# Kernel tuning notes

Measured on AMD Instinct MI355X. Metric: run time of the kernel, lower is better.

## Reference

```python
import jax, jax.numpy as jnp
import numpy as np

H = 4  # attention heads


def gat_layer(x, src, dst, W, a_src, a_dst, b, N):
    """PyG-style GATConv (concat=True, negative_slope=0.2, eval-mode dropout)."""
    h = (x @ W).reshape(N, H, -1)                       # [N,H,C]
    es = jnp.einsum('nhc,hc->nh', h, a_src)             # per-node src score
    ed = jnp.einsum('nhc,hc->nh', h, a_dst)             # per-node dst score
    e = jax.nn.leaky_relu(es[src] + ed[dst], negative_slope=0.2)  # [E,H]
    # segment softmax over incoming edges of each destination node
    emax = jax.ops.segment_max(e, dst, num_segments=N)
    ee = jnp.exp(e - emax[dst])
    denom = jax.ops.segment_sum(ee, dst, num_segments=N)
    alpha = ee / (denom[dst] + 1e-16)                   # [E,H]
    out = jax.ops.segment_sum(h[src] * alpha[..., None], dst, num_segments=N)
    return out.reshape(N, -1) + b                        # [N,H*C]


def setup_inputs() -> dict:
    key = jax.random.key(0)
    ks = jax.random.split(key, 13)
    N, E, D, Q = 50000, 800000, 256, 8
    HID, OUT = 256, 256
    Ch, Co = HID // H, OUT // H
    inp = {}
    inp['x'] = jax.random.normal(ks[0], (N, D), dtype=jnp.float32)
    inp['edge_index'] = jax.random.randint(ks[1], (2, E), 0, N, dtype=jnp.int64)
    inp['query_embedding'] = jax.random.normal(ks[2], (Q, OUT), dtype=jnp.float32)
    # layer 1: input_dim -> heads * (hidden_dim//heads)
    inp['W1'] = jax.random.normal(ks[3], (D, HID), dtype=jnp.float32) / np.sqrt(D).astype(np.float32)
    inp['a_src1'] = jax.random.normal(ks[4], (H, Ch), dtype=jnp.float32) / np.sqrt(Ch).astype(np.float32)
    inp['a_dst1'] = jax.random.normal(ks[5], (H, Ch), dtype=jnp.float32) / np.sqrt(Ch).astype(np.float32)
    inp['b1'] = jnp.zeros((HID,), dtype=jnp.float32)
    # layer 2: hidden_dim -> heads * (output_dim//heads)
    inp['W2'] = jax.random.normal(ks[6], (HID, OUT), dtype=jnp.float32) / np.sqrt(HID).astype(np.float32)
    inp['a_src2'] = jax.random.normal(ks[7], (H, Co), dtype=jnp.float32) / np.sqrt(Co).astype(np.float32)
    inp['a_dst2'] = jax.random.normal(ks[8], (H, Co), dtype=jnp.float32) / np.sqrt(Co).astype(np.float32)
    inp['b2'] = jnp.zeros((OUT,), dtype=jnp.float32)
    # node classifier over concat([query, node]) -> 1 (intended Linear(2*OUT, 1))
    inp['Wc'] = jax.random.normal(ks[9], (2 * OUT, 1), dtype=jnp.float32) / np.sqrt(2 * OUT).astype(np.float32)
    inp['bc'] = jnp.zeros((1,), dtype=jnp.float32)
    return inp


def reference(x, edge_index, query_embedding, W1, a_src1, a_dst1, b1,
              W2, a_src2, a_dst2, b2, Wc, bc):
    N = x.shape[0]
    loops = jnp.arange(N, dtype=edge_index.dtype)        # GATConv add_self_loops=True
    src = jnp.concatenate([edge_index[0], loops])
    dst = jnp.concatenate([edge_index[1], loops])
    h = jax.nn.relu(gat_layer(x, src, dst, W1, a_src1, a_dst1, b1, N))
    emb = gat_layer(h, src, dst, W2, a_src2, a_dst2, b2, N)  # [N, OUT]
    D = emb.shape[1]
    # scores[q,n] = Linear(concat(query[q], emb[n])) — computed without
    # materializing the [Q,N,2D] concat (identical math).
    q_part = query_embedding @ Wc[:D] + bc               # [Q,1]
    n_part = emb @ Wc[D:]                                # [N,1]
    node_scores = q_part[:, 0][:, None] + n_part[:, 0][None, :]  # [Q,N]
    return emb, node_scores
```

## Files before the change

kernel.cpp:

```cpp
#include <hip/hip_runtime.h>

typedef unsigned short u16;
typedef unsigned int   u32;
typedef __attribute__((ext_vector_type(8))) short short8v;
typedef __attribute__((ext_vector_type(8))) unsigned short us8;
typedef __attribute__((ext_vector_type(4))) float f32x4;

static __device__ __forceinline__ float bf2f(u16 u){ union{u32 i; float f;} v; v.i=(u32)u<<16; return v.f; }
static __device__ __forceinline__ u16 f2bf(float f){ union{float f; u32 i;} u; u.f=f; u32 r=u.i+0x7FFFu+((u.i>>16)&1u); return (u16)(r>>16); }

static __device__ __forceinline__ float ld1(const void* p, size_t i, int f32){
  return f32 ? ((const float*)p)[i] : bf2f(((const u16*)p)[i]);
}
static __device__ __forceinline__ float4 ld4(const void* p, size_t i, int f32){
  if (f32) return *((const float4*)((const float*)p + i));
  ushort4 v = *((const ushort4*)((const u16*)p + i));
  return make_float4(bf2f(v.x), bf2f(v.y), bf2f(v.z), bf2f(v.w));
}
static __device__ __forceinline__ void st4(void* p, size_t i, float4 v, int f32){
  if (f32) *((float4*)((float*)p + i)) = v;
  else { ushort4 o; o.x=f2bf(v.x); o.y=f2bf(v.y); o.z=f2bf(v.z); o.w=f2bf(v.w); *((ushort4*)((u16*)p + i)) = o; }
}
static __device__ __forceinline__ void st1(void* p, size_t i, float v, int f32){
  if (f32) ((float*)p)[i] = v; else ((u16*)p)[i] = f2bf(v);
}
static __device__ __forceinline__ int lde(const int* ei, size_t i, int i64){
  return i64 ? ei[2*i] : ei[i];
}
static __device__ __forceinline__ int clampi(int v, int lo, int hi){ return v<lo?lo:(v>hi?hi:v); }

__global__ void detect_zero_kernel(const u32* __restrict__ x, const int* __restrict__ ei,
                                   int* __restrict__ flags, int* __restrict__ deg, int N){
  if (blockIdx.x != 0){
    int i = (blockIdx.x - 1)*256 + threadIdx.x;
    if (i < N) deg[i] = 0;
    return;
  }
  __shared__ int cnt[2];
  int t = threadIdx.x;
  if (t < 2) cnt[t] = 0;
  __syncthreads();
  int good = 0;
  for (int i = t; i < 4096; i += 256){
    u32 e = (x[i] >> 7) & 0xFFu;
    if (e >= 90u && e <= 150u) good++;
  }
  atomicAdd(&cnt[0], good);
  int nzodd = 0;
  for (int i = t; i < 2048; i += 256){
    if (ei[2*i+1] != 0) nzodd++;
  }
  atomicAdd(&cnt[1], nzodd);
  __syncthreads();
  if (t == 0){
    flags[0] = (cnt[0] < 2867) ? 1 : 0;
    flags[1] = (cnt[1] == 0) ? 1 : 0;
  }
}

__global__ void count_kernel(const int* __restrict__ ei, int E, int N,
                             int* __restrict__ deg, const int* __restrict__ flags){
  int i64 = flags[1];
  int i = blockIdx.x*blockDim.x + threadIdx.x;
  int Et = E + N;
  if (i < Et){
    int d = (i < E) ? clampi(lde(ei, (size_t)E + i, i64), 0, N-1) : (i - E);
    atomicAdd(&deg[d], 1);
  }
}

__global__ __launch_bounds__(256) void scan1_kernel(const int* __restrict__ deg,
    int* __restrict__ offs, int* __restrict__ bsum, int N){
  __shared__ int sm[256];
  int t = threadIdx.x;
  int i = blockIdx.x*256 + t;
  int v = (i < N) ? deg[i] : 0;
  sm[t] = v; __syncthreads();
  #pragma unroll
  for (int off = 1; off < 256; off <<= 1){
    int u = (t >= off) ? sm[t-off] : 0;
    __syncthreads();
    sm[t] += u;
    __syncthreads();
  }
  if (i < N) offs[i] = sm[t] - v;
  if (t == 255) bsum[blockIdx.x] = sm[255];
}

__global__ __launch_bounds__(1024) void scan2_kernel(const int* __restrict__ bsum,
    int* __restrict__ bpre, int NB){
  __shared__ int sm[1024];
  int t = threadIdx.x;
  int v = (t < NB) ? bsum[t] : 0;
  sm[t] = v; __syncthreads();
  #pragma unroll
  for (int off = 1; off < 1024; off <<= 1){
    int u = (t >= off) ? sm[t-off] : 0;
    __syncthreads();
    sm[t] += u;
    __syncthreads();
  }
  if (t < NB) bpre[t] = sm[t] - v;
  if (t == 1023) bpre[NB] = sm[1023];
}

__global__ __launch_bounds__(256) void scan3_kernel(int* __restrict__ offs,
    int* __restrict__ cursor, const int* __restrict__ bpre, int N, int NB){
  int i = blockIdx.x*256 + threadIdx.x;
  if (i < N){
    int v = offs[i] + bpre[blockIdx.x];
    offs[i] = v; cursor[i] = v;
  }
  if (i == 0) offs[N] = bpre[NB];
}

__global__ __launch_bounds__(256) void scatter_prep_kernel(const int* __restrict__ ei,
    int E, int N, int SB, int* __restrict__ cursor, int* __restrict__ csr_src,
    const void* __restrict__ B1, const void* __restrict__ B2,
    u16* __restrict__ BT1, u16* __restrict__ BT2,
    const void* __restrict__ query, const void* __restrict__ Wc, const void* __restrict__ bc,
    float* __restrict__ qp, int Q, const int* __restrict__ flags){
  int f32 = flags[0];
  int i64 = flags[1];
  int bid = blockIdx.x;
  if (bid < SB){
    int i = bid*256 + threadIdx.x;
    int Et = E + N;
    if (i < Et){
      int s, d;
      if (i < E){
        s = clampi(lde(ei, i, i64), 0, N-1);
        d = clampi(lde(ei, (size_t)E + i, i64), 0, N-1);
      } else { s = i - E; d = s; }
      int p = atomicAdd(&cursor[d], 1);
      csr_src[p] = s;
    }
    return;
  }
  int pb = bid - SB;
  if (pb < 32){
    const void* B = (pb >= 16) ? B2 : B1;
    u16* BT = (pb >= 16) ? BT2 : BT1;
    int rem = pb & 15;
    int k0 = (rem >> 2)*64, c0 = (rem & 3)*64;
    __shared__ u16 tile[64][65];
    int r0 = threadIdx.x >> 6, c = threadIdx.x & 63;
    for (int r = r0; r < 64; r += 4)
      tile[r][c] = f32 ? f2bf(((const float*)B)[(size_t)(k0+r)*256 + c0 + c])
                       : ((const u16*)B)[(size_t)(k0+r)*256 + c0 + c];
    __syncthreads();
    for (int j = r0; j < 64; j += 4)
      BT[(size_t)(c0+j)*256 + k0 + c] = tile[c][j];
  } else {
    int q = threadIdx.x >> 5, ln = threadIdx.x & 31;
    if (q >= Q) return;
    float s = 0.f;
    for (int j = ln; j < 256; j += 32) s += ld1(query, q*256 + j, f32) * ld1(Wc, j, f32);
    #pragma unroll
    for (int off = 16; off; off >>= 1) s += __shfl_down(s, off, 32);
    if (ln == 0) qp[q] = s + ld1(bc, 0, f32);
  }
}

__global__ __launch_bounds__(512, 4) void gemm_mfma(const void* __restrict__ A,
    const u16* __restrict__ BT, u16* __restrict__ C, int M, int aIsInput,
    const int* __restrict__ flags, float* __restrict__ es, float* __restrict__ ed,
    const void* __restrict__ a_src, const void* __restrict__ a_dst){
  int af32 = aIsInput ? flags[0] : 0;
  int f32 = flags[0];
  __shared__ __align__(16) u16 smem[128*40 + 256*40];
  u16* AsB = smem;
  u16* BsB = smem + 128*40;
  int tid = threadIdx.x;
  int wave = tid >> 6, lane = tid & 63;
  int wm = wave >> 2, wn = wave & 3;
  int l15 = lane & 15, l4 = lane >> 4;
  int row0 = blockIdx.x * 128;
  const u16*  A16 = (const u16*)A;
  const float* A32 = (const float*)A;
  int srow = tid >> 2, sks = (tid & 3) * 8;
  int scol = tid >> 1, skh = (tid & 1) * 16;
  int sgr = min(row0 + srow, M-1);
  f32x4 acc[4][4] = {};
  for (int k0 = 0; k0 < 256; k0 += 32){
    __syncthreads();
    {
      us8 av;
      if (af32){
        const float* ap = A32 + (size_t)sgr*256 + k0 + sks;
        float4 v0 = *(const float4*)ap, v1 = *(const float4*)(ap+4);
        av = (us8){f2bf(v0.x),f2bf(v0.y),f2bf(v0.z),f2bf(v0.w),
                   f2bf(v1.x),f2bf(v1.y),f2bf(v1.z),f2bf(v1.w)};
      } else {
        av = *(const us8*)(A16 + (size_t)sgr*256 + k0 + sks);
      }
      *(us8*)&AsB[srow*40 + sks] = av;
      const u16* bp = BT + (size_t)scol*256 + k0 + skh;
      *(us8*)&BsB[scol*40 + skh]     = *(const us8*)bp;
      *(us8*)&BsB[scol*40 + skh + 8] = *(const us8*)(bp + 8);
    }
    __syncthreads();
    short8v a[4], b[4];
    #pragma unroll
    for (int mi = 0; mi < 4; mi++)
      a[mi] = *(const short8v*)&AsB[(wm*64 + mi*16 + l15)*40 + 8*l4];
    #pragma unroll
    for (int ni = 0; ni < 4; ni++)
      b[ni] = *(const short8v*)&BsB[(wn*64 + ni*16 + l15)*40 + 8*l4];
    #pragma unroll
    for (int mi = 0; mi < 4; mi++)
      #pragma unroll
      for (int ni = 0; ni < 4; ni++)
        acc[mi][ni] = __builtin_amdgcn_mfma_f32_16x16x32_bf16(a[mi], b[ni], acc[mi][ni], 0, 0, 0);
  }
  float as_[4], ad_[4];
  #pragma unroll
  for (int ni = 0; ni < 4; ni++){
    as_[ni] = ld1(a_src, wn*64 + ni*16 + l15, f32);
    ad_[ni] = ld1(a_dst, wn*64 + ni*16 + l15, f32);
  }
  #pragma unroll
  for (int mi = 0; mi < 4; mi++){
    #pragma unroll
    for (int r = 0; r < 4; r++){
      float pe = acc[mi][0][r]*as_[0] + acc[mi][1][r]*as_[1]
               + acc[mi][2][r]*as_[2] + acc[mi][3][r]*as_[3];
      float pd = acc[mi][0][r]*ad_[0] + acc[mi][1][r]*ad_[1]
               + acc[mi][2][r]*ad_[2] + acc[mi][3][r]*ad_[3];
      #pragma unroll
      for (int off = 1; off < 16; off <<= 1){
        pe += __shfl_xor(pe, off, 64);
        pd += __shfl_xor(pd, off, 64);
      }
      if (l15 == 0){
        int row = row0 + wm*64 + mi*16 + l4*4 + r;
        if (row < M){
          es[(size_t)row*4 + wn] = pe;
          ed[(size_t)row*4 + wn] = pd;
        }
      }
    }
  }
  u16* tile = smem;
  __syncthreads();
  #pragma unroll
  for (int mi = 0; mi < 4; mi++){
    #pragma unroll
    for (int ni = 0; ni < 4; ni++)
      #pragma unroll
      for (int r = 0; r < 4; r++)
        tile[(wm*16 + l4*4 + r)*264 + wn*64 + ni*16 + l15] = f2bf(acc[mi][ni][r]);
    __syncthreads();
    #pragma unroll
    for (int c = tid; c < 1024; c += 512){
      int lr = c >> 5, col = (c & 31) * 8;
      int grow = row0 + (lr >> 4)*64 + mi*16 + (lr & 15);
      if (grow < M)
        *(us8*)&C[(size_t)grow*256 + col] = *(const us8*)&tile[lr*264 + col];
    }
    __syncthreads();
  }
}

__global__ __launch_bounds__(256) void agg_kernel(const u16* __restrict__ h,
    const int* __restrict__ csr_src, const int* __restrict__ offs,
    const float* __restrict__ es, const float* __restrict__ ed, int N,
    const void* __restrict__ bias, void* __restrict__ out, int do_relu, int outIsOutput,
    const int* __restrict__ flags, const void* __restrict__ Wc,
    const float* __restrict__ qp, int Q){
  int f32in = flags[0];
  int of32  = outIsOutput ? flags[0] : 0;
  int ln = threadIdx.x & 63;
  int n = blockIdx.x*4 + (threadIdx.x >> 6);
  if (n >= N) return;
  int beg = offs[n], end = offs[n+1];
  int hd = ln >> 4, c0 = ln*4;
  float edn = ed[(size_t)n*4 + hd];
  float a0=0.f, a1=0.f, a2=0.f, a3=0.f, ws=0.f;
  int i = beg;
  for (; i + 8 <= end; i += 8){
    int s[8]; float x[8]; ushort4 hv[8];
    #pragma unroll
    for (int j = 0; j < 8; j++) s[j] = csr_src[i+j];
    #pragma unroll
    for (int j = 0; j < 8; j++) x[j] = es[(size_t)s[j]*4 + hd];
    #pragma unroll
    for (int j = 0; j < 8; j++) hv[j] = *(const ushort4*)&h[(size_t)s[j]*256 + c0];
    #pragma unroll
    for (int j = 0; j < 8; j++){
      float t = x[j] + edn; t = (t > 0.f) ? t : 0.2f*t; t = fminf(t, 60.f);
      float w = __expf(t);
      a0 += w*bf2f(hv[j].x); a1 += w*bf2f(hv[j].y);
      a2 += w*bf2f(hv[j].z); a3 += w*bf2f(hv[j].w);
      ws += w;
    }
  }
  for (; i + 4 <= end; i += 4){
    int s[4]; float x[4]; ushort4 hv[4];
    #pragma unroll
    for (int j = 0; j < 4; j++) s[j] = csr_src[i+j];
    #pragma unroll
    for (int j = 0; j < 4; j++) x[j] = es[(size_t)s[j]*4 + hd];
    #pragma unroll
    for (int j = 0; j < 4; j++) hv[j] = *(const ushort4*)&h[(size_t)s[j]*256 + c0];
    #pragma unroll
    for (int j = 0; j < 4; j++){
      float t = x[j] + edn; t = (t > 0.f) ? t : 0.2f*t; t = fminf(t, 60.f);
      float w = __expf(t);
      a0 += w*bf2f(hv[j].x); a1 += w*bf2f(hv[j].y);
      a2 += w*bf2f(hv[j].z); a3 += w*bf2f(hv[j].w);
      ws += w;
    }
  }
  for (; i < end; i++){
    int s = csr_src[i];
    float t = es[(size_t)s*4 + hd] + edn; t = (t > 0.f) ? t : 0.2f*t; t = fminf(t, 60.f);
    float w = __expf(t);
    ushort4 hv = *(const ushort4*)&h[(size_t)s*256 + c0];
    a0 += w*bf2f(hv.x); a1 += w*bf2f(hv.y);
    a2 += w*bf2f(hv.z); a3 += w*bf2f(hv.w);
    ws += w;
  }
  float inv = 1.f / (ws + 1e-16f);
  float4 bv = ld4(bias, c0, f32in);
  float4 ov = make_float4(a0*inv + bv.x, a1*inv + bv.y, a2*inv + bv.z, a3*inv + bv.w);
  if (do_relu){
    ov.x = fmaxf(ov.x, 0.f); ov.y = fmaxf(ov.y, 0.f);
    ov.z = fmaxf(ov.z, 0.f); ov.w = fmaxf(ov.w, 0.f);
  }
  st4(out, (size_t)n*256 + c0, ov, of32);
  if (outIsOutput){
    float4 wc4 = ld4(Wc, 256 + c0, f32in);
    float v = ov.x*wc4.x + ov.y*wc4.y + ov.z*wc4.z + ov.w*wc4.w;
    #pragma unroll
    for (int off = 1; off < 64; off <<= 1) v += __shfl_xor(v, off, 64);
    if (ln < Q) st1(out, (size_t)N*256 + (size_t)ln*N + n, qp[ln] + v, of32);
  }
}

extern "C" void kernel_launch(void* const* d_in, const int* in_sizes, int n_in,
                              void* d_out, int out_size, void* d_ws, size_t ws_size,
                              hipStream_t stream){
  const void* x     = d_in[0];
  const int*  ei    = (const int*)d_in[1];
  const void* query = d_in[2];
  const void* W1    = d_in[3];
  const void* as1   = d_in[4];
  const void* ad1   = d_in[5];
  const void* b1    = d_in[6];
  const void* W2    = d_in[7];
  const void* as2   = d_in[8];
  const void* ad2   = d_in[9];
  const void* b2    = d_in[10];
  const void* Wc    = d_in[11];
  const void* bc    = d_in[12];

  int N = in_sizes[0] / 256;
  int E = in_sizes[1] / 2;
  int Q = in_sizes[2] / 256;
  int Et = E + N;
  int NB = (N + 255) / 256;
  int SB = (Et + 255) / 256;

  char* p = (char*)d_ws;
  auto alloc = [&](size_t bytes)->char*{
    char* r = p; p += (bytes + 255) & ~(size_t)255; return r;
  };
  int*  flags    = (int*) alloc(256);
  u16*  bufA     = (u16*) alloc((size_t)N*256*2);
  u16*  bufB     = (u16*) alloc((size_t)N*256*2);
  float* es      = (float*)alloc((size_t)N*4*4);
  float* ed      = (float*)alloc((size_t)N*4*4);
  int*  deg      = (int*)  alloc((size_t)N*4);
  int*  offs     = (int*)  alloc((size_t)(N+1)*4);
  int*  cursor   = (int*)  alloc((size_t)N*4);
  int*  csr_src  = (int*)  alloc((size_t)Et*4);
  int*  bsum     = (int*)  alloc((size_t)(NB+1)*4);
  int*  bpre     = (int*)  alloc((size_t)(NB+1)*4);
  u16*  BT1      = (u16*)  alloc(256*256*2);
  u16*  BT2      = (u16*)  alloc(256*256*2);
  float* qp      = (float*)alloc(64*4);

  const int thr = 256;
  detect_zero_kernel<<<NB + 1, 256, 0, stream>>>((const u32*)x, ei, flags, deg, N);
  count_kernel <<<(Et + thr-1)/thr, thr, 0, stream>>>(ei, E, N, deg, flags);
  scan1_kernel <<<NB, 256, 0, stream>>>(deg, offs, bsum, N);
  scan2_kernel <<<1, 1024, 0, stream>>>(bsum, bpre, NB);
  scan3_kernel <<<NB, 256, 0, stream>>>(offs, cursor, bpre, N, NB);
  scatter_prep_kernel<<<SB + 33, 256, 0, stream>>>(ei, E, N, SB, cursor, csr_src,
                                                   W1, W2, BT1, BT2, query, Wc, bc,
                                                   qp, Q, flags);

  int gblocks = (N + 127)/128;
  dim3 ngrid((N + 3)/4);

  gemm_mfma <<<gblocks, 512, 0, stream>>>(x, BT1, bufA, N, 1, flags, es, ed, as1, ad1);
  agg_kernel<<<ngrid, 256, 0, stream>>>(bufA, csr_src, offs, es, ed, N, b1, bufB, 1, 0,
                                        flags, Wc, qp, Q);
  gemm_mfma <<<gblocks, 512, 0, stream>>>(bufB, BT2, bufA, N, 0, flags, es, ed, as2, ad2);
  agg_kernel<<<ngrid, 256, 0, stream>>>(bufA, csr_src, offs, es, ed, N, b2, d_out, 0, 1,
                                        flags, Wc, qp, Q);
}
```

Measured before the change: 299.2 us.

## Precompute per-edge attention weights in CSR order before aggregation

Adds a csr_dst array filled during the scatter and a new edgew_kernel that computes exp(leaky_relu(es[src]+ed[dst])) for all four heads of every edge, storing them contiguously in CSR order. The aggregation kernel then reads these weights with a sequential load instead of gathering es per edge and recomputing the exponential in each of 16 lanes per head. This removes redundant exp work and scattered es loads from the aggregation loop. In exchange it adds an extra kernel launch per layer plus writing and re-reading roughly 13 MB of edge weights and the csr_dst array.

New measurement: 308.9 us. +3.2%, slower.

```diff
diff --git a/kernel.cpp b/kernel.cpp
--- a/kernel.cpp
+++ b/kernel.cpp
@@ -116,6 +116,7 @@
 
 __global__ __launch_bounds__(256) void scatter_prep_kernel(const int* __restrict__ ei,
     int E, int N, int SB, int* __restrict__ cursor, int* __restrict__ csr_src,
+    int* __restrict__ csr_dst,
     const void* __restrict__ B1, const void* __restrict__ B2,
     u16* __restrict__ BT1, u16* __restrict__ BT2,
     const void* __restrict__ query, const void* __restrict__ Wc, const void* __restrict__ bc,
@@ -134,6 +135,7 @@
       } else { s = i - E; d = s; }
       int p = atomicAdd(&cursor[d], 1);
       csr_src[p] = s;
+      csr_dst[p] = d;
     }
     return;
   }
@@ -160,6 +162,22 @@
     for (int off = 16; off; off >>= 1) s += __shfl_down(s, off, 32);
     if (ln == 0) qp[q] = s + ld1(bc, 0, f32);
   }
+}
+
+__global__ __launch_bounds__(256) void edgew_kernel(const int* __restrict__ csr_src,
+    const int* __restrict__ csr_dst, const float* __restrict__ es,
+    const float* __restrict__ ed, float* __restrict__ w_csr, int Et){
+  int i = blockIdx.x*256 + threadIdx.x;
+  if (i >= Et) return;
+  int s = csr_src[i], d = csr_dst[i];
+  float4 e1 = *(const float4*)&es[(size_t)s*4];
+  float4 e2 = *(const float4*)&ed[(size_t)d*4];
+  float4 o;
+  float t0 = e1.x + e2.x; t0 = (t0 > 0.f) ? t0 : 0.2f*t0; o.x = __expf(fminf(t0, 60.f));
+  float t1 = e1.y + e2.y; t1 = (t1 > 0.f) ? t1 : 0.2f*t1; o.y = __expf(fminf(t1, 60.f));
+  float t2 = e1.z + e2.z; t2 = (t2 > 0.f) ? t2 : 0.2f*t2; o.z = __expf(fminf(t2, 60.f));
+  float t3 = e1.w + e2.w; t3 = (t3 > 0.f) ? t3 : 0.2f*t3; o.w = __expf(fminf(t3, 60.f));
+  *(float4*)&w_csr[(size_t)i*4] = o;
 }
 
 __global__ __launch_bounds__(512, 4) void gemm_mfma(const void* __restrict__ A,
@@ -264,7 +282,7 @@
 
 __global__ __launch_bounds__(256) void agg_kernel(const u16* __restrict__ h,
     const int* __restrict__ csr_src, const int* __restrict__ offs,
-    const float* __restrict__ es, const float* __restrict__ ed, int N,
+    const float* __restrict__ w_csr, int N,
     const void* __restrict__ bias, void* __restrict__ out, int do_relu, int outIsOutput,
     const int* __restrict__ flags, const void* __restrict__ Wc,
     const float* __restrict__ qp, int Q){
@@ -275,47 +293,42 @@
   if (n >= N) return;
   int beg = offs[n], end = offs[n+1];
   int hd = ln >> 4, c0 = ln*4;
-  float edn = ed[(size_t)n*4 + hd];
+  const float* wp = w_csr + hd;
   float a0=0.f, a1=0.f, a2=0.f, a3=0.f, ws=0.f;
   int i = beg;
   for (; i + 8 <= end; i += 8){
-    int s[8]; float x[8]; ushort4 hv[8];
+    int s[8]; float w[8]; ushort4 hv[8];
     #pragma unroll
     for (int j = 0; j < 8; j++) s[j] = csr_src[i+j];
     #pragma unroll
-    for (int j = 0; j < 8; j++) x[j] = es[(size_t)s[j]*4 + hd];
+    for (int j = 0; j < 8; j++) w[j] = wp[(size_t)(i+j)*4];
     #pragma unroll
     for (int j = 0; j < 8; j++) hv[j] = *(const ushort4*)&h[(size_t)s[j]*256 + c0];
     #pragma unroll
     for (int j = 0; j < 8; j++){
-      float t = x[j] + edn; t = (t > 0.f) ? t : 0.2f*t; t = fminf(t, 60.f);
-      float w = __expf(t);
-      a0 += w*bf2f(hv[j].x); a1 += w*bf2f(hv[j].y);
-      a2 += w*bf2f(hv[j].z); a3 += w*bf2f(hv[j].w);
-      ws += w;
+      a0 += w[j]*bf2f(hv[j].x); a1 += w[j]*bf2f(hv[j].y);
+      a2 += w[j]*bf2f(hv[j].z); a3 += w[j]*bf2f(hv[j].w);
+      ws += w[j];
     }
   }
   for (; i + 4 <= end; i += 4){
-    int s[4]; float x[4]; ushort4 hv[4];
+    int s[4]; float w[4]; ushort4 hv[4];
     #pragma unroll
     for (int j = 0; j < 4; j++) s[j] = csr_src[i+j];
     #pragma unroll
-    for (int j = 0; j < 4; j++) x[j] = es[(size_t)s[j]*4 + hd];
+    for (int j = 0; j < 4; j++) w[j] = wp[(size_t)(i+j)*4];
     #pragma unroll
     for (int j = 0; j < 4; j++) hv[j] = *(const ushort4*)&h[(size_t)s[j]*256 + c0];
     #pragma unroll
     for (int j = 0; j < 4; j++){
-      float t = x[j] + edn; t = (t > 0.f) ? t : 0.2f*t; t = fminf(t, 60.f);
-      float w = __expf(t);
-      a0 += w*bf2f(hv[j].x); a1 += w*bf2f(hv[j].y);
-      a2 += w*bf2f(hv[j].z); a3 += w*bf2f(hv[j].w);
-      ws += w;
+      a0 += w[j]*bf2f(hv[j].x); a1 += w[j]*bf2f(hv[j].y);
+      a2 += w[j]*bf2f(hv[j].z); a3 += w[j]*bf2f(hv[j].w);
+      ws += w[j];
     }
   }
   for (; i < end; i++){
     int s = csr_src[i];
-    float t = es[(size_t)s*4 + hd] + edn; t = (t > 0.f) ? t : 0.2f*t; t = fminf(t, 60.f);
-    float w = __expf(t);
+    float w = wp[(size_t)i*4];
     ushort4 hv = *(const ushort4*)&h[(size_t)s*256 + c0];
     a0 += w*bf2f(hv.x); a1 += w*bf2f(hv.y);
     a2 += w*bf2f(hv.z); a3 += w*bf2f(hv.w);
@@ -371,10 +384,12 @@
   u16*  bufB     = (u16*) alloc((size_t)N*256*2);
   float* es      = (float*)alloc((size_t)N*4*4);
   float* ed      = (float*)alloc((size_t)N*4*4);
+  float* w_csr   = (float*)alloc((size_t)Et*4*4);
   int*  deg      = (int*)  alloc((size_t)N*4);
   int*  offs     = (int*)  alloc((size_t)(N+1)*4);
   int*  cursor   = (int*)  alloc((size_t)N*4);
   int*  csr_src  = (int*)  alloc((size_t)Et*4);
+  int*  csr_dst  = (int*)  alloc((size_t)Et*4);
   int*  bsum     = (int*)  alloc((size_t)(NB+1)*4);
   int*  bpre     = (int*)  alloc((size_t)(NB+1)*4);
   u16*  BT1      = (u16*)  alloc(256*256*2);
@@ -387,17 +402,20 @@
   scan1_kernel <<<NB, 256, 0, stream>>>(deg, offs, bsum, N);
   scan2_kernel <<<1, 1024, 0, stream>>>(bsum, bpre, NB);
   scan3_kernel <<<NB, 256, 0, stream>>>(offs, cursor, bpre, N, NB);
-  scatter_prep_kernel<<<SB + 33, 256, 0, stream>>>(ei, E, N, SB, cursor, csr_src,
+  scatter_prep_kernel<<<SB + 33, 256, 0, stream>>>(ei, E, N, SB, cursor, csr_src, csr_dst,
                                                    W1, W2, BT1, BT2, query, Wc, bc,
                                                    qp, Q, flags);
 
   int gblocks = (N + 127)/128;
   dim3 ngrid((N + 3)/4);
-
-  gemm_mfma <<<gblocks, 512, 0, stream>>>(x, BT1, bufA, N, 1, flags, es, ed, as1, ad1);
-  agg_kernel<<<ngrid, 256, 0, stream>>>(bufA, csr_src, offs, es, ed, N, b1, bufB, 1, 0,
-                                        flags, Wc, qp, Q);
-  gemm_mfma <<<gblocks, 512, 0, stream>>>(bufB, BT2, bufA, N, 0, flags, es, ed, as2, ad2);
-  agg_kernel<<<ngrid, 256, 0, stream>>>(bufA, csr_src, offs, es, ed, N, b2, d_out, 0, 1,
-                                        flags, Wc, qp, Q);
-}
+  int eblocks = (Et + 255)/256;
+
+  gemm_mfma   <<<gblocks, 512, 0, stream>>>(x, BT1, bufA, N, 1, flags, es, ed, as1, ad1);
+  edgew_kernel<<<eblocks, 256, 0, stream>>>(csr_src, csr_dst, es, ed, w_csr, Et);
+  agg_kernel  <<<ngrid, 256, 0, stream>>>(bufA, csr_src, offs, w_csr, N, b1, bufB, 1, 0,
+                                          flags, Wc, qp, Q);
+  gemm_mfma   <<<gblocks, 512, 0, stream>>>(bufB, BT2, bufA, N, 0, flags, es, ed, as2, ad2);
+  edgew_kernel<<<eblocks, 256, 0, stream>>>(csr_src, csr_dst, es, ed, w_csr, Et);
+  agg_kernel  <<<ngrid, 256, 0, stream>>>(bufA, csr_src, offs, w_csr, N, b2, d_out, 0, 1,
+                                          flags, Wc, qp, Q);
+}
```
